# Performance work log

Measured on AMD Instinct MI355X. Metric: run time of the kernel, lower is better.

## Reference

```python
import jax, jax.numpy as jnp
import numpy as np

jax.config.update("jax_enable_x64", True)  # 64-bit hashes for collision-free WL signatures

N_NODES = 100_000
N_FEATURES = 64
N_EDGES = 6_400_000
NUM_ITERATIONS = 3
STEP = 1


def setup_inputs() -> dict:
    key = jax.random.key(0)
    kx, ke = jax.random.split(key)
    x = jax.random.normal(kx, (N_NODES, N_FEATURES), dtype=jnp.float32)  # one-hot-ish label scores
    edge_index = jax.random.randint(ke, (2, N_EDGES), 0, N_NODES, dtype=jnp.int64)
    return {"x": x, "edge_index": edge_index}


def _splitmix64(z):
    # High-quality 64-bit mixer (uint64, wraps mod 2^64).
    z = z + jnp.uint64(0x9E3779B97F4A7C15)
    z = (z ^ (z >> jnp.uint64(30))) * jnp.uint64(0xBF58476D1CE4E5B9)
    z = (z ^ (z >> jnp.uint64(27))) * jnp.uint64(0x94D049BB133111EB)
    return z ^ (z >> jnp.uint64(31))


def _wl_conv(colors, src, dst, offset):
    """One WL refinement: hash (own color, multiset of neighbor colors), then
    relabel signatures by first-occurrence order (matches PyG WLConv's dict
    insertion order), continuing the global color counter `offset` (matches the
    persistent hashmap across iterations)."""
    n = colors.shape[0]
    h = _splitmix64(colors.astype(jnp.uint64) + jnp.uint64(1))
    # multiset of neighbor colors -> order-invariant sum of neighbor hashes
    nb_sum = jnp.zeros(n, dtype=jnp.uint64).at[dst].add(h[src])  # [N]
    sig = _splitmix64(h * jnp.uint64(0x100000001B3) + nb_sum)    # [N] signatures
    # first-occurrence relabeling (stable, deterministic)
    _, inv = jnp.unique(sig, size=n, fill_value=jnp.uint64(0), return_inverse=True)
    idx = jnp.arange(n, dtype=jnp.int64)
    first_idx = jax.ops.segment_min(idx, inv, num_segments=n)  # empty segments -> int64 max
    order = jnp.argsort(first_idx)                              # real uniques come first
    ranks = jnp.zeros(n, dtype=jnp.int64).at[order].set(idx)
    new_colors = offset + ranks[inv]
    num_new = jnp.sum(first_idx < n).astype(jnp.int64)
    return new_colors, offset + num_new


def reference(x, edge_index):
    src, dst = edge_index[0], edge_index[1]
    colors = jnp.argmax(x, axis=1).astype(jnp.int64)  # [N]
    feats = [colors]
    offset = jnp.int64(0)
    for _ in range(NUM_ITERATIONS):
        for _ in range(STEP):
            colors, offset = _wl_conv(colors, src, dst, offset)
        feats.append(colors)
    return jnp.stack(feats, axis=-1)  # [N, NUM_ITERATIONS+1], int64
```

## Files before the change

kernel.cpp:

```cpp
#include <hip/hip_runtime.h>

typedef unsigned long long u64;
typedef unsigned int u32;

#define TBL_BITS 18
#define TBL_SIZE (1u << TBL_BITS)
#define TBL_MASK (TBL_SIZE - 1u)
#define EMPTY_KEY 0xFFFFFFFFFFFFFFFFull

#define BK_BITS 7
#define BK_SZ   128
#define MAXNB   1024
#define NBLK    256

__device__ __forceinline__ u64 splitmix64(u64 z) {
    z = z + 0x9E3779B97F4A7C15ull;
    z = (z ^ (z >> 30)) * 0xBF58476D1CE4E5B9ull;
    z = (z ^ (z >> 27)) * 0x94D049BB133111EBull;
    return z ^ (z >> 31);
}

__global__ void argmax_kernel(const float* __restrict__ x, u64* __restrict__ h,
                              int* __restrict__ out, u32* __restrict__ offsets, int n) {
    if (blockIdx.x == 0 && threadIdx.x == 0) offsets[0] = 0u;
    int wave = (int)((blockIdx.x * (u32)blockDim.x + threadIdx.x) >> 6);
    int lane = threadIdx.x & 63;
    if (wave >= n) return;
    float v = x[(size_t)wave * 64 + lane];
    int idx = lane;
    #pragma unroll
    for (int off = 32; off >= 1; off >>= 1) {
        float ov = __shfl_xor(v, off);
        int   oi = __shfl_xor(idx, off);
        if (ov > v || (ov == v && oi < idx)) { v = ov; idx = oi; }
    }
    if (lane == 0) {
        h[wave] = splitmix64((u64)idx + 1ull);
        out[(size_t)wave * 4 + 0] = idx;
    }
}


__global__ __launch_bounds__(1024) void count_part(const int* __restrict__ dst,
                                                   u32* __restrict__ cnt, int m, int nbuck) {
    __shared__ u32 hist[MAXNB];
    int t = threadIdx.x, b = blockIdx.x;
    for (int i = t; i < nbuck; i += 1024) hist[i] = 0u;
    __syncthreads();
    int mv = m >> 2;
    int perv = (mv + NBLK - 1) / NBLK;
    int lo = b * perv, hi = lo + perv; if (hi > mv) hi = mv;
    const int4* d4 = (const int4*)dst;
    for (int i = lo + t; i < hi; i += 1024) {
        int4 v = d4[i];
        atomicAdd(&hist[((u32)v.x) >> BK_BITS], 1u);
        atomicAdd(&hist[((u32)v.y) >> BK_BITS], 1u);
        atomicAdd(&hist[((u32)v.z) >> BK_BITS], 1u);
        atomicAdd(&hist[((u32)v.w) >> BK_BITS], 1u);
    }
    if (b == 0 && t == 0)
        for (int e = mv * 4; e < m; ++e) atomicAdd(&hist[((u32)dst[e]) >> BK_BITS], 1u);
    __syncthreads();
    for (int i = t; i < nbuck; i += 1024) cnt[i * NBLK + b] = hist[i];
}

__global__ void scan_bucket(u32* __restrict__ cnt, u32* __restrict__ total, int nbuck) {
    int b = blockIdx.x, t = threadIdx.x;
    u32 v = cnt[b * NBLK + t];
    int lane = t & 63, w = t >> 6;
    int x = (int)v;
    #pragma unroll
    for (int o = 1; o < 64; o <<= 1) {
        int y = __shfl_up(x, o);
        if (lane >= o) x += y;
    }
    __shared__ u32 ws[4];
    if (lane == 63) ws[w] = (u32)x;
    __syncthreads();
    u32 woff = 0;
    for (int ww = 0; ww < w; ++ww) woff += ws[ww];
    u32 incl = woff + (u32)x;
    cnt[b * NBLK + t] = incl - v;
    if (t == 255) total[b] = incl;
}

__global__ __launch_bounds__(1024) void scan_bases(const u32* __restrict__ total,
                                                   u32* __restrict__ bases, int nbuck) {
    __shared__ u32 A[1024], B[1024];
    int t = threadIdx.x;
    u32 pt = (t < nbuck) ? ((total[t] + 63u) & ~63u) : 0u;
    A[t] = pt; __syncthreads();
    u32 *cur = A, *nxt = B;
    for (int o = 1; o < 1024; o <<= 1) {
        u32 y = cur[t] + ((t >= o) ? cur[t - o] : 0u);
        nxt[t] = y; __syncthreads();
        u32* tmp = cur; cur = nxt; nxt = tmp;
    }
    if (t < nbuck) bases[t] = cur[t] - pt;
}

__global__ __launch_bounds__(1024) void scatter_part(const int* __restrict__ src,
                                                     const int* __restrict__ dst,
                                                     const u32* __restrict__ cnt,
                                                     const u32* __restrict__ bases,
                                                     u32* __restrict__ packed, int m, int nbuck) {
    __shared__ u32 pos[MAXNB];
    int t = threadIdx.x, b = blockIdx.x;
    for (int i = t; i < nbuck; i += 1024) pos[i] = bases[i] + cnt[i * NBLK + b];
    __syncthreads();
    int mv = m >> 2;
    int perv = (mv + NBLK - 1) / NBLK;
    int lo = b * perv, hi = lo + perv; if (hi > mv) hi = mv;
    const int4* d4 = (const int4*)dst;
    const int4* s4 = (const int4*)src;
    for (int i = lo + t; i < hi; i += 1024) {
        int4 dv = d4[i]; int4 sv = s4[i];
        u32 d0 = (u32)dv.x, d1 = (u32)dv.y, d2 = (u32)dv.z, d3 = (u32)dv.w;
        u32 p0 = atomicAdd(&pos[d0 >> BK_BITS], 1u);
        packed[p0] = ((u32)sv.x << BK_BITS) | (d0 & (BK_SZ - 1u));
        u32 p1 = atomicAdd(&pos[d1 >> BK_BITS], 1u);
        packed[p1] = ((u32)sv.y << BK_BITS) | (d1 & (BK_SZ - 1u));
        u32 p2 = atomicAdd(&pos[d2 >> BK_BITS], 1u);
        packed[p2] = ((u32)sv.z << BK_BITS) | (d2 & (BK_SZ - 1u));
        u32 p3 = atomicAdd(&pos[d3 >> BK_BITS], 1u);
        packed[p3] = ((u32)sv.w << BK_BITS) | (d3 & (BK_SZ - 1u));
    }
    if (b == 0 && t == 0) {
        for (int e = mv * 4; e < m; ++e) {
            u32 d = (u32)dst[e];
            u32 p = atomicAdd(&pos[d >> BK_BITS], 1u);
            packed[p] = ((u32)src[e] << BK_BITS) | (d & (BK_SZ - 1u));
        }
    }
}

__global__ __launch_bounds__(256) void nb_kernel(const u32* __restrict__ packed,
                                                 const u32* __restrict__ bases,
                                                 const u32* __restrict__ total,
                                                 const u64* __restrict__ h,
                                                 u64* __restrict__ nb,
                                                 u64* __restrict__ keys,
                                                 u32* __restrict__ vals, int n, int nbuck) {
    int b = blockIdx.x, t = threadIdx.x;
    if (b >= nbuck) {
        int base = (b - nbuck) * 1024;
        for (int k = t; k < 1024; k += 256) { keys[base + k] = EMPTY_KEY; vals[base + k] = 0xFFFFFFFFu; }
        return;
    }
    __shared__ u64 acc[BK_SZ];
    if (t < BK_SZ) acc[t] = 0ull;
    __syncthreads();
    u32 lo = bases[b];
    u32 len = total[b];
    const uint4* p4 = (const uint4*)(packed + lo);
    int len4 = (int)(len >> 2);
    for (int i = t; i < len4; i += 256) {
        uint4 v = p4[i];
        atomicAdd(&acc[v.x & (BK_SZ - 1u)], h[v.x >> BK_BITS]);
        atomicAdd(&acc[v.y & (BK_SZ - 1u)], h[v.y >> BK_BITS]);
        atomicAdd(&acc[v.z & (BK_SZ - 1u)], h[v.z >> BK_BITS]);
        atomicAdd(&acc[v.w & (BK_SZ - 1u)], h[v.w >> BK_BITS]);
    }
    for (int e = len4 * 4 + t; e < (int)len; e += 256) {
        u32 v = packed[lo + e];
        atomicAdd(&acc[v & (BK_SZ - 1u)], h[v >> BK_BITS]);
    }
    __syncthreads();
    if (t < BK_SZ) {
        int node = (b << BK_BITS) + t;
        if (node < n) nb[node] = acc[t];
    }
}


__global__ void sig_kernel(const u64* __restrict__ h, const u64* __restrict__ nb,
                           u32* __restrict__ slotarr, u64* __restrict__ keys,
                           u32* __restrict__ vals, int n) {
    int i = blockIdx.x * blockDim.x + threadIdx.x;
    if (i >= n) return;
    u64 s = splitmix64(h[i] * 0x100000001B3ull + nb[i]);
    u32 slot = (u32)s & TBL_MASK;
    while (true) {
        u64 prev = atomicCAS(&keys[slot], (u64)EMPTY_KEY, s);
        if (prev == EMPTY_KEY || prev == s) break;
        slot = (slot + 1u) & TBL_MASK;
    }
    atomicMin(&vals[slot], (u32)i);
    slotarr[i] = slot;
}

__global__ void count_rank(const u32* __restrict__ slotarr, const u32* __restrict__ vals,
                           u32* __restrict__ f, u32* __restrict__ lrank,
                           u32* __restrict__ partials, int n) {
    int b = blockIdx.x, t = threadIdx.x;
    int i = b * 256 + t;
    u32 isf = 0, fi = 0;
    if (i < n) {
        fi = vals[slotarr[i]];
        f[i] = fi;
        isf = (fi == (u32)i) ? 1u : 0u;
    }
    __shared__ u32 wsum[4];
    u32 lane = t & 63, wv = (u32)t >> 6;
    int x = (int)isf;
    #pragma unroll
    for (int o = 1; o < 64; o <<= 1) {
        int y = __shfl_up(x, o);
        if (lane >= (u32)o) x += y;
    }
    if (lane == 63) wsum[wv] = (u32)x;
    __syncthreads();
    u32 woff = 0;
    for (u32 w = 0; w < wv; ++w) woff += wsum[w];
    if (i < n) lrank[i] = woff + (u32)x - isf;
    if (t == 255) partials[b] = woff + (u32)x;
}

__global__ void scan_partials(const u32* __restrict__ partials, u32* __restrict__ pp,
                              u32* __restrict__ offsets, int iter, int nblk) {
    __shared__ u32 A[512], B[512];
    int t = threadIdx.x;
    u32 v = (t < nblk) ? partials[t] : 0u;
    A[t] = v; __syncthreads();
    u32 *cur = A, *nxt = B;
    for (int o = 1; o < 512; o <<= 1) {
        u32 y = cur[t] + ((t >= o) ? cur[t - o] : 0u);
        nxt[t] = y; __syncthreads();
        u32* tmp = cur; cur = nxt; nxt = tmp;
    }
    if (t < nblk) pp[t] = cur[t] - v;
    if (t == 511) offsets[iter + 1] = offsets[iter] + cur[511];
}

__global__ void relabel_fast(const u32* __restrict__ f, const u32* __restrict__ lrank,
                             const u32* __restrict__ pp, const u32* __restrict__ offsets,
                             int iter, u64* __restrict__ h, int* __restrict__ out, int n) {
    int i = blockIdx.x * 256 + threadIdx.x;
    if (i >= n) return;
    u32 j = f[i];
    u32 c = offsets[iter] + pp[j >> 8] + lrank[j];
    h[i] = splitmix64((u64)c + 1ull);
    out[(size_t)i * 4 + (iter + 1)] = (int)c;
}


__global__ void init_iter_kernel(u64* __restrict__ keys, u32* __restrict__ vals,
                                 u64* __restrict__ nb, int n) {
    int i = blockIdx.x * blockDim.x + threadIdx.x;
    if (i < (int)TBL_SIZE) { keys[i] = EMPTY_KEY; vals[i] = 0xFFFFFFFFu; }
    if (i < n) nb[i] = 0ull;
}

__global__ void edge_kernel(const int* __restrict__ src, const int* __restrict__ dst,
                            const u64* __restrict__ h, u64* __restrict__ nb, int m) {
    int stride = gridDim.x * blockDim.x;
    for (int e = blockIdx.x * blockDim.x + threadIdx.x; e < m; e += stride) {
        atomicAdd(&nb[(u32)dst[e]], h[(u32)src[e]]);
    }
}

extern "C" void kernel_launch(void* const* d_in, const int* in_sizes, int n_in,
                              void* d_out, int out_size, void* d_ws, size_t ws_size,
                              hipStream_t stream) {
    const float* x = (const float*)d_in[0];
    const int* ei = (const int*)d_in[1];
    int n = in_sizes[0] / 64;
    int m = in_sizes[1] / 2;
    const int* src = ei;
    const int* dst = ei + m;
    int* out = (int*)d_out;

    const int NPB = (n + 255) / 256;
    const int nbuck = (n + BK_SZ - 1) >> BK_BITS;

    auto align = [](size_t v) { return (v + 255) & ~(size_t)255; };
    size_t sz_packed = align((size_t)m * 4 + (size_t)MAXNB * 64 * 4);
    size_t sz_cnt    = align((size_t)MAXNB * NBLK * 4);
    size_t sz_bt     = align((size_t)MAXNB * 4);
    size_t sz_h      = align((size_t)n * 8);
    size_t sz_tblk   = align((size_t)TBL_SIZE * 8);
    size_t sz_tblv   = align((size_t)TBL_SIZE * 4);
    size_t sz_n4     = align((size_t)n * 4);
    size_t sz_small  = align((size_t)512 * 4);
    size_t need_fast = sz_packed + sz_cnt + 2 * sz_bt + 2 * sz_h + sz_tblk + sz_tblv
                     + 3 * sz_n4 + 2 * sz_small + 256;

    char* p = (char*)d_ws;
    bool fast = (ws_size >= need_fast) && (nbuck <= MAXNB) && ((m & 3) == 0) && (NPB <= 512);
    if (fast) {
        u32* packed  = (u32*)p; p += sz_packed;
        u32* cnt     = (u32*)p; p += sz_cnt;
        u32* total   = (u32*)p; p += sz_bt;
        u32* bases   = (u32*)p; p += sz_bt;
        u64* h       = (u64*)p; p += sz_h;
        u64* nb      = (u64*)p; p += sz_h;
        u64* keys    = (u64*)p; p += sz_tblk;
        u32* vals    = (u32*)p; p += sz_tblv;
        u32* slotarr = (u32*)p; p += sz_n4;
        u32* f       = (u32*)p; p += sz_n4;
        u32* lrank   = (u32*)p; p += sz_n4;
        u32* partials= (u32*)p; p += sz_small;
        u32* pp      = (u32*)p; p += sz_small;
        u32* offsets = (u32*)p;

        argmax_kernel<<<(n + 3) / 4, 256, 0, stream>>>(x, h, out, offsets, n);
        count_part  <<<NBLK, 1024, 0, stream>>>(dst, cnt, m, nbuck);
        scan_bucket <<<nbuck, 256, 0, stream>>>(cnt, total, nbuck);
        scan_bases  <<<1, 1024, 0, stream>>>(total, bases, nbuck);
        scatter_part<<<NBLK, 1024, 0, stream>>>(src, dst, cnt, bases, packed, m, nbuck);

        for (int it = 0; it < 3; ++it) {
            nb_kernel    <<<nbuck + 256, 256, 0, stream>>>(packed, bases, total, h, nb, keys, vals, n, nbuck);
            sig_kernel   <<<NPB, 256, 0, stream>>>(h, nb, slotarr, keys, vals, n);
            count_rank   <<<NPB, 256, 0, stream>>>(slotarr, vals, f, lrank, partials, n);
            scan_partials<<<1, 512, 0, stream>>>(partials, pp, offsets, it, NPB);
            relabel_fast <<<NPB, 256, 0, stream>>>(f, lrank, pp, offsets, it, h, out, n);
        }
    } else {
        u64* h       = (u64*)p; p += sz_h;
        u64* nb      = (u64*)p; p += sz_h;
        u64* keys    = (u64*)p; p += sz_tblk;
        u32* vals    = (u32*)p; p += sz_tblv;
        u32* slotarr = (u32*)p; p += sz_n4;
        u32* f       = (u32*)p; p += sz_n4;
        u32* lrank   = (u32*)p; p += sz_n4;
        u32* partials= (u32*)p; p += sz_small;
        u32* pp      = (u32*)p; p += sz_small;
        u32* offsets = (u32*)p;

        argmax_kernel<<<(n + 3) / 4, 256, 0, stream>>>(x, h, out, offsets, n);
        for (int it = 0; it < 3; ++it) {
            init_iter_kernel<<<(TBL_SIZE + 255) / 256, 256, 0, stream>>>(keys, vals, nb, n);
            edge_kernel  <<<4096, 256, 0, stream>>>(src, dst, h, nb, m);
            sig_kernel   <<<NPB, 256, 0, stream>>>(h, nb, slotarr, keys, vals, n);
            count_rank   <<<NPB, 256, 0, stream>>>(slotarr, vals, f, lrank, partials, n);
            scan_partials<<<1, 512, 0, stream>>>(partials, pp, offsets, it, NPB);
            relabel_fast <<<NPB, 256, 0, stream>>>(f, lrank, pp, offsets, it, h, out, n);
        }
    }
}
```

Baseline: 256.6 us.

## Use larger dst buckets split across four sub-blocks with partial sums

Buckets grow from 128 to 512 destination nodes (196 buckets instead of 782), and each bucket's edge range is split across four blocks. Each block writes its partial neighbor sums to a separate strided buffer, and the signature kernel adds the four partials. The hash-table probe now reads the key before attempting a CAS, which avoids atomics on slots that are already occupied. The aim is to cut scatter-phase bucket atomics and spread the aggregation evenly across blocks. The cost is four times the nb storage and extra reads in the signature kernel.

```diff
diff --git a/kernel.cpp b/kernel.cpp
--- a/kernel.cpp
+++ b/kernel.cpp
@@ -8,10 +8,11 @@
 #define TBL_MASK (TBL_SIZE - 1u)
 #define EMPTY_KEY 0xFFFFFFFFFFFFFFFFull
 
-#define BK_BITS 7
-#define BK_SZ   128
-#define MAXNB   1024
+#define BK_BITS 9
+#define BK_SZ   512
+#define MAXNB   256
 #define NBLK    256
+#define NSUB    4
 
 __device__ __forceinline__ u64 splitmix64(u64 z) {
     z = z + 0x9E3779B97F4A7C15ull;
@@ -84,14 +85,13 @@
     if (t == 255) total[b] = incl;
 }
 
-__global__ __launch_bounds__(1024) void scan_bases(const u32* __restrict__ total,
-                                                   u32* __restrict__ bases, int nbuck) {
-    __shared__ u32 A[1024], B[1024];
+__global__ void scan_bases(const u32* __restrict__ total, u32* __restrict__ bases, int nbuck) {
+    __shared__ u32 A[256], B[256];
     int t = threadIdx.x;
     u32 pt = (t < nbuck) ? ((total[t] + 63u) & ~63u) : 0u;
     A[t] = pt; __syncthreads();
     u32 *cur = A, *nxt = B;
-    for (int o = 1; o < 1024; o <<= 1) {
+    for (int o = 1; o < 256; o <<= 1) {
         u32 y = cur[t] + ((t >= o) ? cur[t - o] : 0u);
         nxt[t] = y; __syncthreads();
         u32* tmp = cur; cur = nxt; nxt = tmp;
@@ -138,51 +138,69 @@
                                                  const u32* __restrict__ bases,
                                                  const u32* __restrict__ total,
                                                  const u64* __restrict__ h,
-                                                 u64* __restrict__ nb,
+                                                 u64* __restrict__ nb4, size_t nstride,
                                                  u64* __restrict__ keys,
-                                                 u32* __restrict__ vals, int n, int nbuck) {
+                                                 u32* __restrict__ vals, int nbuck) {
     int b = blockIdx.x, t = threadIdx.x;
-    if (b >= nbuck) {
-        int base = (b - nbuck) * 1024;
+    if (b >= nbuck * NSUB) {
+        int base = (b - nbuck * NSUB) * 1024;
         for (int k = t; k < 1024; k += 256) { keys[base + k] = EMPTY_KEY; vals[base + k] = 0xFFFFFFFFu; }
         return;
     }
+    int bucket = b >> 2, sub = b & 3;
     __shared__ u64 acc[BK_SZ];
-    if (t < BK_SZ) acc[t] = 0ull;
-    __syncthreads();
-    u32 lo = bases[b];
-    u32 len = total[b];
-    const uint4* p4 = (const uint4*)(packed + lo);
-    int len4 = (int)(len >> 2);
-    for (int i = t; i < len4; i += 256) {
-        uint4 v = p4[i];
-        atomicAdd(&acc[v.x & (BK_SZ - 1u)], h[v.x >> BK_BITS]);
-        atomicAdd(&acc[v.y & (BK_SZ - 1u)], h[v.y >> BK_BITS]);
-        atomicAdd(&acc[v.z & (BK_SZ - 1u)], h[v.z >> BK_BITS]);
-        atomicAdd(&acc[v.w & (BK_SZ - 1u)], h[v.w >> BK_BITS]);
-    }
-    for (int e = len4 * 4 + t; e < (int)len; e += 256) {
-        u32 v = packed[lo + e];
+    acc[t] = 0ull; acc[t + 256] = 0ull;
+    __syncthreads();
+    u32 lo = bases[bucket];
+    u32 len = total[bucket];
+    u32 q0 = (len * (u32)sub) >> 2;
+    u32 q1 = (len * (u32)(sub + 1)) >> 2;
+    for (u32 e = lo + q0 + (u32)t; e < lo + q1; e += 256) {
+        u32 v = packed[e];
         atomicAdd(&acc[v & (BK_SZ - 1u)], h[v >> BK_BITS]);
     }
     __syncthreads();
-    if (t < BK_SZ) {
-        int node = (b << BK_BITS) + t;
-        if (node < n) nb[node] = acc[t];
-    }
-}
-
-
-__global__ void sig_kernel(const u64* __restrict__ h, const u64* __restrict__ nb,
-                           u32* __restrict__ slotarr, u64* __restrict__ keys,
-                           u32* __restrict__ vals, int n) {
+    u64* dst = nb4 + (size_t)sub * nstride + ((size_t)bucket << BK_BITS);
+    dst[t] = acc[t];
+    dst[t + 256] = acc[t + 256];
+}
+
+
+__global__ void sig_kernel4(const u64* __restrict__ h, const u64* __restrict__ nb4,
+                            size_t nstride, u32* __restrict__ slotarr,
+                            u64* __restrict__ keys, u32* __restrict__ vals, int n) {
+    int i = blockIdx.x * blockDim.x + threadIdx.x;
+    if (i >= n) return;
+    u64 nbv = nb4[i] + nb4[nstride + i] + nb4[2 * nstride + i] + nb4[3 * nstride + i];
+    u64 s = splitmix64(h[i] * 0x100000001B3ull + nbv);
+    u32 slot = (u32)s & TBL_MASK;
+    while (true) {
+        u64 k = keys[slot];
+        if (k == s) break;
+        if (k == EMPTY_KEY) {
+            u64 prev = atomicCAS(&keys[slot], (u64)EMPTY_KEY, s);
+            if (prev == EMPTY_KEY || prev == s) break;
+        }
+        slot = (slot + 1u) & TBL_MASK;
+    }
+    atomicMin(&vals[slot], (u32)i);
+    slotarr[i] = slot;
+}
+
+__global__ void sig_kernel1(const u64* __restrict__ h, const u64* __restrict__ nb,
+                            u32* __restrict__ slotarr, u64* __restrict__ keys,
+                            u32* __restrict__ vals, int n) {
     int i = blockIdx.x * blockDim.x + threadIdx.x;
     if (i >= n) return;
     u64 s = splitmix64(h[i] * 0x100000001B3ull + nb[i]);
     u32 slot = (u32)s & TBL_MASK;
     while (true) {
-        u64 prev = atomicCAS(&keys[slot], (u64)EMPTY_KEY, s);
-        if (prev == EMPTY_KEY || prev == s) break;
+        u64 k = keys[slot];
+        if (k == s) break;
+        if (k == EMPTY_KEY) {
+            u64 prev = atomicCAS(&keys[slot], (u64)EMPTY_KEY, s);
+            if (prev == EMPTY_KEY || prev == s) break;
+        }
         slot = (slot + 1u) & TBL_MASK;
     }
     atomicMin(&vals[slot], (u32)i);
@@ -272,17 +290,19 @@
 
     const int NPB = (n + 255) / 256;
     const int nbuck = (n + BK_SZ - 1) >> BK_BITS;
+    const size_t nstride = (size_t)nbuck << BK_BITS;
 
     auto align = [](size_t v) { return (v + 255) & ~(size_t)255; };
     size_t sz_packed = align((size_t)m * 4 + (size_t)MAXNB * 64 * 4);
     size_t sz_cnt    = align((size_t)MAXNB * NBLK * 4);
     size_t sz_bt     = align((size_t)MAXNB * 4);
     size_t sz_h      = align((size_t)n * 8);
+    size_t sz_nb4    = align(nstride * 8 * NSUB);
     size_t sz_tblk   = align((size_t)TBL_SIZE * 8);
     size_t sz_tblv   = align((size_t)TBL_SIZE * 4);
     size_t sz_n4     = align((size_t)n * 4);
     size_t sz_small  = align((size_t)512 * 4);
-    size_t need_fast = sz_packed + sz_cnt + 2 * sz_bt + 2 * sz_h + sz_tblk + sz_tblv
+    size_t need_fast = sz_packed + sz_cnt + 2 * sz_bt + sz_h + sz_nb4 + sz_tblk + sz_tblv
                      + 3 * sz_n4 + 2 * sz_small + 256;
 
     char* p = (char*)d_ws;
@@ -293,7 +313,7 @@
         u32* total   = (u32*)p; p += sz_bt;
         u32* bases   = (u32*)p; p += sz_bt;
         u64* h       = (u64*)p; p += sz_h;
-        u64* nb      = (u64*)p; p += sz_h;
+        u64* nb4     = (u64*)p; p += sz_nb4;
         u64* keys    = (u64*)p; p += sz_tblk;
         u32* vals    = (u32*)p; p += sz_tblv;
         u32* slotarr = (u32*)p; p += sz_n4;
@@ -306,12 +326,13 @@
         argmax_kernel<<<(n + 3) / 4, 256, 0, stream>>>(x, h, out, offsets, n);
         count_part  <<<NBLK, 1024, 0, stream>>>(dst, cnt, m, nbuck);
         scan_bucket <<<nbuck, 256, 0, stream>>>(cnt, total, nbuck);
-        scan_bases  <<<1, 1024, 0, stream>>>(total, bases, nbuck);
+        scan_bases  <<<1, 256, 0, stream>>>(total, bases, nbuck);
         scatter_part<<<NBLK, 1024, 0, stream>>>(src, dst, cnt, bases, packed, m, nbuck);
 
         for (int it = 0; it < 3; ++it) {
-            nb_kernel    <<<nbuck + 256, 256, 0, stream>>>(packed, bases, total, h, nb, keys, vals, n, nbuck);
-            sig_kernel   <<<NPB, 256, 0, stream>>>(h, nb, slotarr, keys, vals, n);
+            nb_kernel    <<<nbuck * NSUB + 256, 256, 0, stream>>>(packed, bases, total, h,
+                                                                  nb4, nstride, keys, vals, nbuck);
+            sig_kernel4  <<<NPB, 256, 0, stream>>>(h, nb4, nstride, slotarr, keys, vals, n);
             count_rank   <<<NPB, 256, 0, stream>>>(slotarr, vals, f, lrank, partials, n);
             scan_partials<<<1, 512, 0, stream>>>(partials, pp, offsets, it, NPB);
             relabel_fast <<<NPB, 256, 0, stream>>>(f, lrank, pp, offsets, it, h, out, n);
@@ -332,7 +353,7 @@
         for (int it = 0; it < 3; ++it) {
             init_iter_kernel<<<(TBL_SIZE + 255) / 256, 256, 0, stream>>>(keys, vals, nb, n);
             edge_kernel  <<<4096, 256, 0, stream>>>(src, dst, h, nb, m);
-            sig_kernel   <<<NPB, 256, 0, stream>>>(h, nb, slotarr, keys, vals, n);
+            sig_kernel1  <<<NPB, 256, 0, stream>>>(h, nb, slotarr, keys, vals, n);
             count_rank   <<<NPB, 256, 0, stream>>>(slotarr, vals, f, lrank, partials, n);
             scan_partials<<<1, 512, 0, stream>>>(partials, pp, offsets, it, NPB);
             relabel_fast <<<NPB, 256, 0, stream>>>(f, lrank, pp, offsets, it, h, out, n);
```

Measured after the change: 251.6 us. 2.0% less time.
